# Kernel optimization log

Hardware: AMD Instinct MI355X
Metric: run time of the kernel (lower is better)

## Reference

```python
import jax, jax.numpy as jnp
import numpy as np

N, E, T = 10000, 160000, 1200000
D, DM, H, L, Z = 256, 64, 1024, 3, 100


def setup_inputs() -> dict:
    key = jax.random.key(0)
    ks = jax.random.split(key, 24)
    rn = lambda k, shp, s: (s * jax.random.normal(k, shp)).astype(jnp.float32)
    return {
        'atomic_number': jax.random.randint(ks[0], (N,), 1, Z),
        'g_src': jax.random.randint(ks[1], (E,), 0, N),
        'g_dst': jax.random.randint(ks[2], (E,), 0, N),
        't_src': jax.random.randint(ks[3], (T,), 0, E),
        't_dst': jax.random.randint(ks[4], (T,), 0, E),
        'r': rn(ks[5], (E, 3), 1.5),  # bond displacement vectors, |r| ~ 2.4 A
        'atom_emb': rn(ks[6], (Z, D), 0.05),
        'Wsrc': rn(ks[7], (L, D, DM), 0.05), 'bsrc': rn(ks[8], (L, DM), 0.05),
        'Wdst': rn(ks[9], (L, D, DM), 0.05), 'bdst': rn(ks[10], (L, DM), 0.05),
        'Wedge': rn(ks[11], (L, D, DM), 0.05), 'bedge': rn(ks[12], (L, DM), 0.05),
        'attn': rn(ks[13], (L, DM), 0.05),
        'W1': rn(ks[14], (L, DM, H), 0.05), 'b1': rn(ks[15], (L, H), 0.05),
        'W2': rn(ks[16], (L, H, D), 0.05), 'b2': rn(ks[17], (L, D), 0.05),
        'Wfc': rn(ks[18], (D, 1), 0.05), 'bfc': rn(ks[19], (1,), 0.05),
    }


def _forward(atomic_number, g_src, g_dst, t_src, t_dst, r, atom_emb,
             Wsrc, bsrc, Wdst, bdst, Wedge, bedge, attn, W1, b1, W2, b2, Wfc, bfc):
    n_nodes = atomic_number.shape[0]
    n_edges = r.shape[0]
    d_model = atom_emb.shape[1]
    channels = attn.shape[-1]

    # atom embedding + RBF bond encoding (vmin=0, vmax=8, bins=d_model)
    x = atom_emb[atomic_number]                       # [N, D]
    bondlength = jnp.linalg.norm(r, axis=1)           # [E]
    centers = jnp.linspace(0.0, 8.0, d_model)
    gamma = 1.0 / (centers[1] - centers[0]) ** 2
    y = jnp.exp(-gamma * (bondlength[:, None] - centers[None, :]) ** 2)  # [E, D]

    # angular (Chebyshev) features on triplet graph t; t.ndata['r'] = g.edata['r']
    rnorm = -r / bondlength[:, None]                  # [E, 3]
    cos_jik = jnp.sum(rnorm[t_src] * rnorm[t_dst], axis=1)  # [T]
    kc = jnp.arange(channels, dtype=cos_jik.dtype)
    theta = jnp.arccos(jnp.clip(cos_jik, -1.0, 1.0))
    z_jik = jnp.cos(kc[None, :] * theta[:, None])     # [T, C] Chebyshev T_k(cos)

    node_idx = g_dst[t_dst]                           # triplet -> destination atom

    for l in range(Wsrc.shape[0]):
        xj = x @ Wsrc[l] + bsrc[l]                    # [N, DM]
        xi = x @ Wdst[l] + bdst[l]                    # [N, DM]
        xij = xj[g_src] + xi[g_dst] + (y @ Wedge[l] + bedge[l])  # [E, DM]

        e_jik = jax.nn.silu(z_jik + xij[t_src] + xij[t_dst])     # [T, DM]
        logit = jnp.sum(e_jik * attn[l], axis=-1)                # [T]
        # edge_softmax grouped by destination bond (t_dst)
        m = jax.ops.segment_max(logit, t_dst, num_segments=n_edges)
        ex = jnp.exp(logit - m[t_dst])
        den = jax.ops.segment_sum(ex, t_dst, num_segments=n_edges)
        a = ex / den[t_dst]                                      # [T]

        # scatter attended messages to destination atoms
        ft = jax.ops.segment_sum(a[:, None] * xij[t_src], node_idx,
                                 num_segments=n_nodes)           # [N, DM]
        # feedforward: DM -> 4*D -> D
        x = jax.nn.silu(ft @ W1[l] + b1[l]) @ W2[l] + b2[l]      # [N, D]

    atomwise_energy = x @ Wfc + bfc                   # [N, 1]
    return jnp.squeeze(jnp.mean(atomwise_energy))     # AvgPooling, eV/atom


def reference(atomic_number, g_src, g_dst, t_src, t_dst, r, atom_emb,
              Wsrc, bsrc, Wdst, bdst, Wedge, bedge, attn, W1, b1, W2, b2, Wfc, bfc):
    return _forward(atomic_number, g_src, g_dst, t_src, t_dst, r, atom_emb,
                    Wsrc, bsrc, Wdst, bdst, Wedge, bedge, attn, W1, b1, W2, b2, Wfc, bfc)
```

## Files before the change

kernel.cpp:

```cpp
#include <hip/hip_runtime.h>
#include <math.h>


#define DM 64
#define DMODEL 256
#define HDIM 1024
#define WPAD 264

#define BSH 9
#define NBMAX 320
#define CAPB 4608

typedef unsigned short bf16_t;
typedef __attribute__((ext_vector_type(8))) short s8v;
typedef __attribute__((ext_vector_type(4))) float f4;

__device__ __forceinline__ bf16_t f2bf(float f) {
    unsigned int u = __float_as_uint(f);
    return (bf16_t)((u + 0x7FFFu + ((u >> 16) & 1u)) >> 16);
}
__device__ __forceinline__ float bf_lo(unsigned int u) {
    return __uint_as_float(u << 16);
}
__device__ __forceinline__ float bf_hi(unsigned int u) {
    return __uint_as_float(u & 0xFFFF0000u);
}
__device__ __forceinline__ float bf2f(bf16_t v) {
    return __uint_as_float((unsigned int)v << 16);
}
__device__ __forceinline__ float silu_f(float u) {
    return u * __builtin_amdgcn_rcpf(1.f + __expf(-u));
}

__global__ void k_embed(const int* __restrict__ an, const float* __restrict__ emb,
                        bf16_t* __restrict__ x) {
    int n = blockIdx.x;
    int d = threadIdx.x;
    x[n * DMODEL + d] = f2bf(emb[an[n] * DMODEL + d]);
}

__global__ void k_edge_geom(const float* __restrict__ r, float* __restrict__ bl,
                            float* __restrict__ rn, int E) {
    int e = blockIdx.x * blockDim.x + threadIdx.x;
    if (e >= E) return;
    float a = r[e * 3 + 0], b = r[e * 3 + 1], c = r[e * 3 + 2];
    float l = sqrtf(a * a + b * b + c * c);
    bl[e] = l;
    float inv = 1.0f / l;
    rn[e * 3 + 0] = a * inv;
    rn[e * 3 + 1] = b * inv;
    rn[e * 3 + 2] = c * inv;
}

__global__ void k_hist(const int* __restrict__ idx, int* __restrict__ cnt, int M) {
    int t = blockIdx.x * blockDim.x + threadIdx.x;
    if (t < M) atomicAdd(&cnt[idx[t]], 1);
}

__global__ __launch_bounds__(256) void k_scan_part(
    const int* __restrict__ cnt, int* __restrict__ bsum, int M) {
    __shared__ int sm[4];
    int tid = threadIdx.x;
    int i = blockIdx.x * 256 + tid;
    int v = (i < M) ? cnt[i] : 0;
    for (int off = 32; off > 0; off >>= 1) v += __shfl_xor(v, off, 64);
    if ((tid & 63) == 0) sm[tid >> 6] = v;
    __syncthreads();
    if (tid == 0) bsum[blockIdx.x] = sm[0] + sm[1] + sm[2] + sm[3];
}

__global__ __launch_bounds__(1024) void k_scan_mid(int* __restrict__ bsum, int nb) {
    __shared__ int sm[1024];
    int tid = threadIdx.x;
    int v = (tid < nb) ? bsum[tid] : 0;
    sm[tid] = v;
    __syncthreads();
    for (int off = 1; off < 1024; off <<= 1) {
        int u = (tid >= off) ? sm[tid - off] : 0;
        __syncthreads();
        sm[tid] += u;
        __syncthreads();
    }
    if (tid < nb) bsum[tid] = sm[tid] - v;
}

__global__ __launch_bounds__(256) void k_scan_final(
    const int* __restrict__ cnt, const int* __restrict__ bsum,
    int* __restrict__ rowp, int M, int total) {
    __shared__ int sm[256];
    int tid = threadIdx.x;
    int i = blockIdx.x * 256 + tid;
    int v = (i < M) ? cnt[i] : 0;
    sm[tid] = v;
    __syncthreads();
    for (int off = 1; off < 256; off <<= 1) {
        int u = (tid >= off) ? sm[tid - off] : 0;
        __syncthreads();
        sm[tid] += u;
        __syncthreads();
    }
    if (i < M) rowp[i] = bsum[blockIdx.x] + sm[tid] - v;
    if (i == 0) rowp[M] = total;
}


__global__ __launch_bounds__(512) void k_bhist(
    const int* __restrict__ td, int* __restrict__ gbcnt, int T, int NB) {
    __shared__ int h[NBMAX];
    int tid = threadIdx.x;
    for (int i = tid; i < NBMAX; i += 512) h[i] = 0;
    __syncthreads();
    int t0 = blockIdx.x * 4096;
    #pragma unroll
    for (int i = 0; i < 8; ++i) {
        int t = t0 + tid + i * 512;
        if (t < T) atomicAdd(&h[td[t] >> BSH], 1);
    }
    __syncthreads();
    for (int b = tid; b < NB; b += 512)
        if (h[b]) atomicAdd(&gbcnt[b], h[b]);
}

__global__ __launch_bounds__(512) void k_bscan(
    const int* __restrict__ gbcnt, int* __restrict__ bbase, int NB, int total) {
    __shared__ int sm[512];
    int tid = threadIdx.x;
    int v = (tid < NB) ? gbcnt[tid] : 0;
    sm[tid] = v;
    __syncthreads();
    for (int off = 1; off < 512; off <<= 1) {
        int u = (tid >= off) ? sm[tid - off] : 0;
        __syncthreads();
        sm[tid] += u;
        __syncthreads();
    }
    if (tid < NB) bbase[tid] = sm[tid] - v;
    if (tid == 0) bbase[NB] = total;
}

__global__ __launch_bounds__(512) void k_passA(
    const int* __restrict__ ts, const int* __restrict__ td,
    const float* __restrict__ rn, const int* __restrict__ bbase,
    int* __restrict__ bcur, int2* __restrict__ ipair, float* __restrict__ idv,
    int T, int NB) {
    __shared__ int   std_[4096];
    __shared__ int   ssrc[4096];
    __shared__ float sdv[4096];
    __shared__ int lbcnt[NBMAX], lbase[NBMAX], lpos[NBMAX], lgst[NBMAX],
                   lbb[NBMAX];
    __shared__ int ssc[512];
    int tid = threadIdx.x;
    int t0 = blockIdx.x * 4096;
    int total = min(4096, T - t0);
    for (int i = tid; i < NBMAX; i += 512) lbcnt[i] = 0;
    for (int i = tid; i < NB; i += 512) lbb[i] = bbase[i];
    __syncthreads();
    int   mtd[8], msrc[8];
    float md[8];
    #pragma unroll
    for (int i = 0; i < 8; ++i) {
        int idx = tid + i * 512;
        mtd[i] = -1;
        if (idx < total) {
            int t = t0 + idx;
            int a = ts[t], b = td[t];
            float d = rn[a * 3 + 0] * rn[b * 3 + 0]
                    + rn[a * 3 + 1] * rn[b * 3 + 1]
                    + rn[a * 3 + 2] * rn[b * 3 + 2];
            d = fminf(1.0f, fmaxf(-1.0f, d));
            mtd[i] = b; msrc[i] = a; md[i] = d;
            atomicAdd(&lbcnt[b >> BSH], 1);
        }
    }
    __syncthreads();
    int v = (tid < NB) ? lbcnt[tid] : 0;
    ssc[tid] = v;
    __syncthreads();
    for (int off = 1; off < 512; off <<= 1) {
        int u = (tid >= off) ? ssc[tid - off] : 0;
        __syncthreads();
        ssc[tid] += u;
        __syncthreads();
    }
    if (tid < NB) {
        int ex = ssc[tid] - v;
        lbase[tid] = ex;
        lpos[tid] = ex;
    }
    __syncthreads();
    #pragma unroll
    for (int i = 0; i < 8; ++i) {
        if (mtd[i] >= 0) {
            int bin = mtd[i] >> BSH;
            int p = atomicAdd(&lpos[bin], 1);
            std_[p] = mtd[i]; ssrc[p] = msrc[i]; sdv[p] = md[i];
        }
    }
    __syncthreads();
    for (int b = tid; b < NB; b += 512)
        if (lbcnt[b]) lgst[b] = atomicAdd(&bcur[b], lbcnt[b]);
    __syncthreads();
    for (int j = tid; j < total; j += 512) {
        int bin = std_[j] >> BSH;
        int dest = lbb[bin] + lgst[bin] + (j - lbase[bin]);
        ipair[dest] = make_int2(std_[j], ssrc[j]);
        idv[dest] = sdv[j];
    }
}

__global__ __launch_bounds__(512) void k_passB(
    const int2* __restrict__ ipair, const float* __restrict__ idv,
    const int* __restrict__ bbase, int2* __restrict__ packed,
    int* __restrict__ rowp, int E, int T) {
    __shared__ int2 spk[CAPB];
    __shared__ int hcnt[512], lcur[512], ssc[512];
    int tid = threadIdx.x;
    int b = blockIdx.x;
    int ibeg = bbase[b], iend = bbase[b + 1];
    int nb = iend - ibeg;
    int e0 = b << BSH;
    hcnt[tid] = 0;
    __syncthreads();
    for (int j = ibeg + tid; j < iend; j += 512)
        atomicAdd(&hcnt[ipair[j].x - e0], 1);
    __syncthreads();
    int v = hcnt[tid];
    ssc[tid] = v;
    __syncthreads();
    for (int off = 1; off < 512; off <<= 1) {
        int u = (tid >= off) ? ssc[tid - off] : 0;
        __syncthreads();
        ssc[tid] += u;
        __syncthreads();
    }
    int excl = ssc[tid] - v;
    lcur[tid] = excl;
    int e = e0 + tid;
    if (e < E) rowp[e] = ibeg + excl;
    if (b == 0 && tid == 0) rowp[E] = T;
    __syncthreads();
    bool staged = (nb <= CAPB);
    for (int j = ibeg + tid; j < iend; j += 512) {
        int2 pr = ipair[j];
        int pos = atomicAdd(&lcur[pr.x - e0], 1);
        int2 out = make_int2(pr.y, __float_as_int(idv[j]));
        if (staged) spk[pos] = out;
        else packed[ibeg + pos] = out;
    }
    __syncthreads();
    if (staged)
        for (int j = tid; j < nb; j += 512) packed[ibeg + j] = spk[j];
}

__global__ void k_escatter(const int* __restrict__ gd, const int* __restrict__ erowp,
                           int* __restrict__ cursor, int* __restrict__ eord, int E) {
    int e = blockIdx.x * blockDim.x + threadIdx.x;
    if (e >= E) return;
    int n = gd[e];
    int pos = erowp[n] + atomicAdd(&cursor[n], 1);
    eord[pos] = e;
}

__global__ __launch_bounds__(256) void k_deghist(
    const int* __restrict__ rowp, int* __restrict__ dcnt, int E) {
    __shared__ int h[256];
    int tid = threadIdx.x;
    h[tid] = 0;
    __syncthreads();
    int e = blockIdx.x * 256 + tid;
    if (e < E) {
        int d = rowp[e + 1] - rowp[e];
        if (d > 255) d = 255;
        atomicAdd(&h[d], 1);
    }
    __syncthreads();
    if (h[tid]) atomicAdd(&dcnt[tid], h[tid]);
}

__global__ __launch_bounds__(256) void k_degscatter(
    const int* __restrict__ rowp, const int* __restrict__ doff,
    int* __restrict__ dcur, int* __restrict__ eperm, int E) {
    __shared__ int lcnt[256];
    __shared__ int base[256];
    int tid = threadIdx.x;
    lcnt[tid] = 0;
    __syncthreads();
    int e = blockIdx.x * 256 + tid;
    int d = 0, rk = 0;
    if (e < E) {
        d = rowp[e + 1] - rowp[e];
        if (d > 255) d = 255;
        rk = atomicAdd(&lcnt[d], 1);
    }
    __syncthreads();
    if (lcnt[tid]) base[tid] = atomicAdd(&dcur[tid], lcnt[tid]);
    __syncthreads();
    if (e < E) eperm[E - 1 - (doff[d] + base[d] + rk)] = e;
}

__global__ __launch_bounds__(256) void k_castT(
    const float* __restrict__ src, bf16_t* __restrict__ dst, int K, int Nn) {
    __shared__ float tile[32][33];
    int k0 = blockIdx.x * 32, n0 = blockIdx.y * 32;
    int tx = threadIdx.x & 31, ty = threadIdx.x >> 5;
    #pragma unroll
    for (int i = 0; i < 4; ++i) {
        int row = ty + i * 8;
        tile[row][tx] = src[(size_t)(k0 + row) * Nn + n0 + tx];
    }
    __syncthreads();
    #pragma unroll
    for (int i = 0; i < 4; ++i) {
        int row = ty + i * 8;
        dst[(size_t)(n0 + row) * K + k0 + tx] = f2bf(tile[tx][row]);
    }
}

__global__ __launch_bounds__(256) void k_node_proj(
    const bf16_t* __restrict__ xb,
    const bf16_t* __restrict__ Wst, const float* __restrict__ bs,
    const bf16_t* __restrict__ Wdt, const float* __restrict__ bd,
    bf16_t* __restrict__ xs, bf16_t* __restrict__ xd, int N) {
    __shared__ bf16_t wsl[64 * WPAD];
    __shared__ bf16_t wdl[64 * WPAD];
    int tid = threadIdx.x;
    for (int i = tid; i < 2048; i += 256) {
        int row = i >> 5, inw = i & 31;
        *(uint4*)&wsl[row * WPAD + inw * 8] =
            *(const uint4*)&Wst[(size_t)row * DMODEL + inw * 8];
        *(uint4*)&wdl[row * WPAD + inw * 8] =
            *(const uint4*)&Wdt[(size_t)row * DMODEL + inw * 8];
    }
    __syncthreads();
    int w = tid >> 6, lane = tid & 63;
    int col = lane & 15, quad = lane >> 4;
    int m0 = blockIdx.x * 64 + w * 16;
    f4 as[4] = {{0.f,0.f,0.f,0.f},{0.f,0.f,0.f,0.f},
                {0.f,0.f,0.f,0.f},{0.f,0.f,0.f,0.f}};
    f4 ad[4] = {{0.f,0.f,0.f,0.f},{0.f,0.f,0.f,0.f},
                {0.f,0.f,0.f,0.f},{0.f,0.f,0.f,0.f}};
    #pragma unroll
    for (int k0 = 0; k0 < DMODEL; k0 += 32) {
        s8v a = *(const s8v*)&xb[(size_t)(m0 + col) * DMODEL + k0 + quad * 8];
        #pragma unroll
        for (int t = 0; t < 4; ++t) {
            s8v b1v = *(const s8v*)&wsl[(t * 16 + col) * WPAD + k0 + quad * 8];
            as[t] = __builtin_amdgcn_mfma_f32_16x16x32_bf16(a, b1v, as[t], 0, 0, 0);
            s8v b2v = *(const s8v*)&wdl[(t * 16 + col) * WPAD + k0 + quad * 8];
            ad[t] = __builtin_amdgcn_mfma_f32_16x16x32_bf16(a, b2v, ad[t], 0, 0, 0);
        }
    }
    #pragma unroll
    for (int t = 0; t < 4; ++t) {
        int c = t * 16 + col;
        float bsv = bs[c], bdv = bd[c];
        #pragma unroll
        for (int r = 0; r < 4; ++r) {
            int m = m0 + quad * 4 + r;
            if (m < N) {
                xs[(size_t)m * DM + c] = f2bf(as[t][r] + bsv);
                xd[(size_t)m * DM + c] = f2bf(ad[t][r] + bdv);
            }
        }
    }
}

__global__ __launch_bounds__(256) void k_xij(
    const float* __restrict__ bl, const bf16_t* __restrict__ Wedgt,
    const float* __restrict__ be,
    const bf16_t* __restrict__ xs, const bf16_t* __restrict__ xd,
    const int* __restrict__ gs, const int* __restrict__ gd,
    bf16_t* __restrict__ xij, int E) {
    __shared__ bf16_t wel[64 * WPAD];
    int tid = threadIdx.x;
    for (int i = tid; i < 2048; i += 256) {
        int row = i >> 5, inw = i & 31;
        *(uint4*)&wel[row * WPAD + inw * 8] =
            *(const uint4*)&Wedgt[(size_t)row * DMODEL + inw * 8];
    }
    __syncthreads();
    int w = tid >> 6, lane = tid & 63;
    int col = lane & 15, quad = lane >> 4;
    int m0 = blockIdx.x * 64 + w * 16;
    const float step = 8.0f / 255.0f;
    const float gamma = (255.0f / 8.0f) * (255.0f / 8.0f);
    int me = m0 + col;
    float blv = (me < E) ? bl[me] : 0.f;
    f4 acc[4] = {{0.f,0.f,0.f,0.f},{0.f,0.f,0.f,0.f},
                 {0.f,0.f,0.f,0.f},{0.f,0.f,0.f,0.f}};
    #pragma unroll
    for (int k0 = 0; k0 < DMODEL; k0 += 32) {
        s8v a;
        #pragma unroll
        for (int j = 0; j < 8; ++j) {
            float c = (float)(k0 + quad * 8 + j) * step;
            float dd = blv - c;
            a[j] = (short)f2bf(__expf(-gamma * dd * dd));
        }
        #pragma unroll
        for (int t = 0; t < 4; ++t) {
            s8v b = *(const s8v*)&wel[(t * 16 + col) * WPAD + k0 + quad * 8];
            acc[t] = __builtin_amdgcn_mfma_f32_16x16x32_bf16(a, b, acc[t], 0, 0, 0);
        }
    }
    #pragma unroll
    for (int r = 0; r < 4; ++r) {
        int e = m0 + quad * 4 + r;
        if (e >= E) continue;
        int s = gs[e], d2 = gd[e];
        #pragma unroll
        for (int t = 0; t < 4; ++t) {
            int c = t * 16 + col;
            float v = acc[t][r] + bf2f(xs[(size_t)s * DM + c])
                    + bf2f(xd[(size_t)d2 * DM + c]) + be[c];
            xij[(size_t)e * DM + c] = f2bf(v);
        }
    }
}

__global__ __launch_bounds__(256) void k_edge_attn(
    const bf16_t* __restrict__ xij, const int2* __restrict__ packed,
    const int* __restrict__ rowp, const float* __restrict__ attn_l,
    const int* __restrict__ eperm, bf16_t* __restrict__ msg, int E) {
    int gtid = blockIdx.x * 256 + threadIdx.x;
    int ei = gtid >> 2;
    if (ei >= E) return;
    int q = gtid & 3;
    int e = eperm[ei];
    int beg = rowp[e], end = rowp[e + 1];

    float av[16];
    #pragma unroll
    for (int c = 0; c < 16; ++c) av[c] = attn_l[q * 16 + c];

    uint4 xe0, xe1;
    {
        const uint4* xer = (const uint4*)&xij[(size_t)e * DM + q * 16];
        xe0 = xer[0]; xe1 = xer[1];
    }
    float acc[16];
    #pragma unroll
    for (int c = 0; c < 16; ++c) acc[c] = 0.f;
    float den = 0.f;

    int degw = __builtin_amdgcn_readfirstlane(end - beg);
    if (degw > 9) __builtin_amdgcn_s_setprio(1);

    if (beg < end) {
        int2 pk0 = packed[beg];
        int2 pk1 = (beg + 1 < end) ? packed[beg + 1] : pk0;
        const uint4* s0 = (const uint4*)&xij[(size_t)pk0.x * DM + q * 16];
        uint4 nsa = s0[0], nsb = s0[1];
        for (int p = beg; p < end; ++p) {
            float d = __int_as_float(pk0.y);
            uint4 xa = nsa, xb = nsb;
            if (p + 1 < end) {
                const uint4* sn = (const uint4*)&xij[(size_t)pk1.x * DM + q * 16];
                nsa = sn[0]; nsb = sn[1];
                pk0 = pk1;
                if (p + 2 < end) pk1 = packed[p + 2];
            }
            float d2 = d + d;
            float t2  = fmaf(d2, d, -1.f);
            float t3  = fmaf(d2, t2, -d);
            float t4  = fmaf(t2 + t2, t2, -1.f);
            float t7  = fmaf(t4 + t4, t3, -d);
            float t8  = fmaf(t4 + t4, t4, -1.f);
            float t15 = fmaf(t8 + t8, t7, -d);
            float t16 = fmaf(t8 + t8, t8, -1.f);
            float t17 = fmaf(t16 + t16, d, -t15);
            float t31 = fmaf(t16 + t16, t15, -d);
            float t32 = fmaf(t16 + t16, t16, -1.f);
            float t33 = fmaf(t32 + t32, d, -t31);
            float t48 = fmaf(t32 + t32, t16, -t16);
            float t49 = fmaf(t32 + t32, t17, -t15);
            float za, zb;
            if (q == 0)      { za = 1.f;  zb = d;   }
            else if (q == 1) { za = t16;  zb = t17; }
            else if (q == 2) { za = t32;  zb = t33; }
            else             { za = t48;  zb = t49; }
            float logit = 0.f;
            #define CH2(uw, ew, c)                                            \
            {                                                                 \
                float u0 = za + bf_lo(uw) + bf_lo(ew);                        \
                float zn = fmaf(d2, zb, -za); za = zb; zb = zn;               \
                float u1 = za + bf_hi(uw) + bf_hi(ew);                        \
                zn = fmaf(d2, zb, -za); za = zb; zb = zn;                     \
                logit = fmaf(silu_f(u0), av[c], logit);                       \
                logit = fmaf(silu_f(u1), av[c + 1], logit);                   \
            }
            CH2(xa.x, xe0.x, 0);
            CH2(xa.y, xe0.y, 2);
            CH2(xa.z, xe0.z, 4);
            CH2(xa.w, xe0.w, 6);
            CH2(xb.x, xe1.x, 8);
            CH2(xb.y, xe1.y, 10);
            CH2(xb.z, xe1.z, 12);
            CH2(xb.w, xe1.w, 14);
            #undef CH2
            logit += __shfl_xor(logit, 1, 64);
            logit += __shfl_xor(logit, 2, 64);
            float wg = __expf(logit);
            den += wg;
            acc[0]  = fmaf(wg, bf_lo(xa.x), acc[0]);
            acc[1]  = fmaf(wg, bf_hi(xa.x), acc[1]);
            acc[2]  = fmaf(wg, bf_lo(xa.y), acc[2]);
            acc[3]  = fmaf(wg, bf_hi(xa.y), acc[3]);
            acc[4]  = fmaf(wg, bf_lo(xa.z), acc[4]);
            acc[5]  = fmaf(wg, bf_hi(xa.z), acc[5]);
            acc[6]  = fmaf(wg, bf_lo(xa.w), acc[6]);
            acc[7]  = fmaf(wg, bf_hi(xa.w), acc[7]);
            acc[8]  = fmaf(wg, bf_lo(xb.x), acc[8]);
            acc[9]  = fmaf(wg, bf_hi(xb.x), acc[9]);
            acc[10] = fmaf(wg, bf_lo(xb.y), acc[10]);
            acc[11] = fmaf(wg, bf_hi(xb.y), acc[11]);
            acc[12] = fmaf(wg, bf_lo(xb.z), acc[12]);
            acc[13] = fmaf(wg, bf_hi(xb.z), acc[13]);
            acc[14] = fmaf(wg, bf_lo(xb.w), acc[14]);
            acc[15] = fmaf(wg, bf_hi(xb.w), acc[15]);
        }
    }
    __builtin_amdgcn_s_setprio(0);
    float inv = (den > 0.f) ? 1.f / den : 0.f;
    uint4 o0, o1;
    o0.x = (unsigned int)f2bf(acc[0] * inv)  | ((unsigned int)f2bf(acc[1] * inv) << 16);
    o0.y = (unsigned int)f2bf(acc[2] * inv)  | ((unsigned int)f2bf(acc[3] * inv) << 16);
    o0.z = (unsigned int)f2bf(acc[4] * inv)  | ((unsigned int)f2bf(acc[5] * inv) << 16);
    o0.w = (unsigned int)f2bf(acc[6] * inv)  | ((unsigned int)f2bf(acc[7] * inv) << 16);
    o1.x = (unsigned int)f2bf(acc[8] * inv)  | ((unsigned int)f2bf(acc[9] * inv) << 16);
    o1.y = (unsigned int)f2bf(acc[10] * inv) | ((unsigned int)f2bf(acc[11] * inv) << 16);
    o1.z = (unsigned int)f2bf(acc[12] * inv) | ((unsigned int)f2bf(acc[13] * inv) << 16);
    o1.w = (unsigned int)f2bf(acc[14] * inv) | ((unsigned int)f2bf(acc[15] * inv) << 16);
    uint4* op = (uint4*)&msg[(size_t)e * DM + q * 16];
    op[0] = o0;
    op[1] = o1;
}

__global__ __launch_bounds__(256) void k_aggregate(
    const bf16_t* __restrict__ msg, const int* __restrict__ erowp,
    const int* __restrict__ eord, bf16_t* __restrict__ ft, int N) {
    int gtid = blockIdx.x * 256 + threadIdx.x;
    int n = gtid >> 4;
    if (n >= N) return;
    int quad = gtid & 15;
    int beg = erowp[n], end = erowp[n + 1];
    float a0 = 0.f, a1 = 0.f, a2 = 0.f, a3 = 0.f;
    for (int j = beg; j < end; ++j) {
        uint2 uv = *(const uint2*)&msg[(size_t)eord[j] * DM + quad * 4];
        a0 += bf_lo(uv.x); a1 += bf_hi(uv.x);
        a2 += bf_lo(uv.y); a3 += bf_hi(uv.y);
    }
    ushort4 o = {f2bf(a0), f2bf(a1), f2bf(a2), f2bf(a3)};
    *(ushort4*)&ft[(size_t)n * DM + quad * 4] = o;
}

__global__ __launch_bounds__(256) void k_ffn_fused(
    const bf16_t* __restrict__ ft, const bf16_t* __restrict__ W1t,
    const float* __restrict__ b1, const bf16_t* __restrict__ W2t,
    const float* __restrict__ b2, bf16_t* __restrict__ x, int N) {
    __shared__ bf16_t w1s[2][64 * 72];
    __shared__ bf16_t w2s[2][64 * 72];
    __shared__ bf16_t hld[4][16 * 72];
    __shared__ float b1s[HDIM];
    int tid = threadIdx.x;
    int w = tid >> 6, lane = tid & 63;
    int col = lane & 15, quad = lane >> 4;
    int m0 = blockIdx.x * 64 + w * 16;
    int c0 = blockIdx.y * 64;
    bf16_t* myl = hld[w];

    #pragma unroll
    for (int j = 0; j < 4; ++j) b1s[tid + j * 256] = b1[tid + j * 256];

    s8v fa0 = *(const s8v*)&ft[(size_t)(m0 + col) * DM + quad * 8];
    s8v fa1 = *(const s8v*)&ft[(size_t)(m0 + col) * DM + 32 + quad * 8];

    int srow0 = tid >> 3;
    int srow1 = 32 + srow0;
    int skb = tid & 7;

    f4 acc[4] = {{0.f,0.f,0.f,0.f},{0.f,0.f,0.f,0.f},
                 {0.f,0.f,0.f,0.f},{0.f,0.f,0.f,0.f}};

    {
        uint4 a0 = *(const uint4*)&W1t[(size_t)srow0 * DM + skb * 8];
        uint4 a1 = *(const uint4*)&W1t[(size_t)srow1 * DM + skb * 8];
        uint4 c0v = *(const uint4*)&W2t[(size_t)(c0 + srow0) * HDIM + skb * 8];
        uint4 c1v = *(const uint4*)&W2t[(size_t)(c0 + srow1) * HDIM + skb * 8];
        *(uint4*)&w1s[0][srow0 * 72 + skb * 8] = a0;
        *(uint4*)&w1s[0][srow1 * 72 + skb * 8] = a1;
        *(uint4*)&w2s[0][srow0 * 72 + skb * 8] = c0v;
        *(uint4*)&w2s[0][srow1 * 72 + skb * 8] = c1v;
    }
    __syncthreads();

    #pragma unroll 1
    for (int kc = 0; kc < 16; ++kc) {
        int cb = kc & 1, nb = cb ^ 1;
        int ch0 = kc * 64;
        int chn = (kc < 15) ? ch0 + 64 : ch0;
        uint4 na0 = *(const uint4*)&W1t[(size_t)(chn + srow0) * DM + skb * 8];
        uint4 na1 = *(const uint4*)&W1t[(size_t)(chn + srow1) * DM + skb * 8];
        uint4 nc0 = *(const uint4*)&W2t[(size_t)(c0 + srow0) * HDIM + chn + skb * 8];
        uint4 nc1 = *(const uint4*)&W2t[(size_t)(c0 + srow1) * HDIM + chn + skb * 8];
        #pragma unroll
        for (int th = 0; th < 4; ++th) {
            s8v wb0 = *(const s8v*)&w1s[cb][(th * 16 + col) * 72 + quad * 8];
            s8v wb1 = *(const s8v*)&w1s[cb][(th * 16 + col) * 72 + 32 + quad * 8];
            f4 hv = {0.f, 0.f, 0.f, 0.f};
            hv = __builtin_amdgcn_mfma_f32_16x16x32_bf16(fa0, wb0, hv, 0, 0, 0);
            hv = __builtin_amdgcn_mfma_f32_16x16x32_bf16(fa1, wb1, hv, 0, 0, 0);
            float bb = b1s[ch0 + th * 16 + col];
            #pragma unroll
            for (int r = 0; r < 4; ++r)
                myl[(quad * 4 + r) * 72 + th * 16 + col] =
                    f2bf(silu_f(hv[r] + bb));
        }
        s8v ha0 = *(const s8v*)&myl[col * 72 + quad * 8];
        s8v ha1 = *(const s8v*)&myl[col * 72 + 32 + quad * 8];
        #pragma unroll
        for (int t2 = 0; t2 < 4; ++t2) {
            s8v vb0 = *(const s8v*)&w2s[cb][(t2 * 16 + col) * 72 + quad * 8];
            s8v vb1 = *(const s8v*)&w2s[cb][(t2 * 16 + col) * 72 + 32 + quad * 8];
            acc[t2] = __builtin_amdgcn_mfma_f32_16x16x32_bf16(ha0, vb0, acc[t2], 0, 0, 0);
            acc[t2] = __builtin_amdgcn_mfma_f32_16x16x32_bf16(ha1, vb1, acc[t2], 0, 0, 0);
        }
        __syncthreads();
        if (kc < 15) {
            *(uint4*)&w1s[nb][srow0 * 72 + skb * 8] = na0;
            *(uint4*)&w1s[nb][srow1 * 72 + skb * 8] = na1;
            *(uint4*)&w2s[nb][srow0 * 72 + skb * 8] = nc0;
            *(uint4*)&w2s[nb][srow1 * 72 + skb * 8] = nc1;
        }
        __syncthreads();
    }
    #pragma unroll
    for (int t2 = 0; t2 < 4; ++t2) {
        int c = c0 + t2 * 16 + col;
        float bb = b2[c];
        #pragma unroll
        for (int r = 0; r < 4; ++r) {
            int m = m0 + quad * 4 + r;
            if (m < N) x[(size_t)m * DMODEL + c] = f2bf(acc[t2][r] + bb);
        }
    }
}

__global__ __launch_bounds__(256) void k_out_reduce(
    const bf16_t* __restrict__ x, const float* __restrict__ Wfc,
    float* __restrict__ acc, int NT) {
    __shared__ float sm[4];
    int tid = threadIdx.x;
    float v = 0.f;
    int np = NT / 2;
    const unsigned int* xp = (const unsigned int*)x;
    for (int i = blockIdx.x * blockDim.x + tid; i < np; i += gridDim.x * blockDim.x) {
        unsigned int u = xp[i];
        int c = (2 * i) & (DMODEL - 1);
        v = fmaf(bf_lo(u), Wfc[c], v);
        v = fmaf(bf_hi(u), Wfc[c + 1], v);
    }
    for (int off = 32; off > 0; off >>= 1) v += __shfl_xor(v, off, 64);
    if ((tid & 63) == 0) sm[tid >> 6] = v;
    __syncthreads();
    if (tid == 0) {
        float s = sm[0] + sm[1] + sm[2] + sm[3];
        atomicAdd(acc, s);
    }
}

__global__ void k_out_final(const float* __restrict__ acc, const float* __restrict__ bfc,
                            float* __restrict__ out, float invN) {
    out[0] = acc[0] * invN + bfc[0];
}

extern "C" void kernel_launch(void* const* d_in, const int* in_sizes, int n_in,
                              void* d_out, int out_size, void* d_ws, size_t ws_size,
                              hipStream_t stream) {
    const int*   an    = (const int*)d_in[0];
    const int*   gs    = (const int*)d_in[1];
    const int*   gd    = (const int*)d_in[2];
    const int*   ts    = (const int*)d_in[3];
    const int*   td    = (const int*)d_in[4];
    const float* r     = (const float*)d_in[5];
    const float* emb   = (const float*)d_in[6];
    const float* Wsrc  = (const float*)d_in[7];
    const float* bsrc  = (const float*)d_in[8];
    const float* Wdst  = (const float*)d_in[9];
    const float* bdst  = (const float*)d_in[10];
    const float* Wedge = (const float*)d_in[11];
    const float* bedge = (const float*)d_in[12];
    const float* attn  = (const float*)d_in[13];
    const float* W1    = (const float*)d_in[14];
    const float* b1    = (const float*)d_in[15];
    const float* W2    = (const float*)d_in[16];
    const float* b2    = (const float*)d_in[17];
    const float* Wfc   = (const float*)d_in[18];
    const float* bfc   = (const float*)d_in[19];

    const int N = in_sizes[0];
    const int E = in_sizes[1];
    const int T = in_sizes[3];
    const int NB = (E + 511) >> BSH;

    char* w = (char*)d_ws;
    size_t off = 0;
    auto alloc = [&](size_t bytes) {
        void* p = w + off;
        off += (bytes + 255) & ~(size_t)255;
        return p;
    };
    bf16_t* xb     = (bf16_t*)alloc((size_t)(N + 64) * DMODEL * 2);
    float*  rn     = (float*) alloc((size_t)E * 3 * 4);
    float*  bl     = (float*) alloc(((size_t)E + 64) * 4);
    int*    rowp   = (int*)   alloc(((size_t)E + 1) * 4);
    int*    bsum   = (int*)   alloc(4096);
    int2*   packed = (int2*)  alloc((size_t)T * 8);
    int2*   ipair  = (int2*)  alloc((size_t)T * 8);
    float*  idv    = (float*) alloc((size_t)T * 4);
    int*    gbcnt  = (int*)   alloc(NBMAX * 4);
    int*    bbase  = (int*)   alloc((NBMAX + 1) * 4);
    int*    bcur   = (int*)   alloc(NBMAX * 4);
    int*    ecnt   = (int*)   alloc((size_t)N * 4);
    int*    erowp  = (int*)   alloc(((size_t)N + 1) * 4);
    int*    eord   = (int*)   alloc((size_t)E * 4);
    int*    eperm  = (int*)   alloc((size_t)E * 4);
    int*    dcnt   = (int*)   alloc(1024);
    int*    dcur   = (int*)   alloc(1024);
    bf16_t* xs     = (bf16_t*)alloc((size_t)N * DM * 2);
    bf16_t* xd     = (bf16_t*)alloc((size_t)N * DM * 2);
    bf16_t* xij    = (bf16_t*)alloc((size_t)E * DM * 2);
    bf16_t* msg    = (bf16_t*)alloc((size_t)E * DM * 2);
    bf16_t* ft     = (bf16_t*)alloc((size_t)(N + 64) * DM * 2);
    bf16_t* W1t    = (bf16_t*)alloc((size_t)3 * HDIM * DM * 2);
    bf16_t* W2t    = (bf16_t*)alloc((size_t)3 * DMODEL * HDIM * 2);
    bf16_t* Wedgt  = (bf16_t*)alloc((size_t)3 * DM * DMODEL * 2);
    bf16_t* Wst    = (bf16_t*)alloc((size_t)3 * DM * DMODEL * 2);
    bf16_t* Wdt    = (bf16_t*)alloc((size_t)3 * DM * DMODEL * 2);
    float*  accs   = (float*) alloc(64);
    (void)ws_size; (void)n_in; (void)out_size;

    const int nbScanN = (N + 255) / 256;
    const int nbT = (T + 4095) / 4096;

    k_embed<<<N, 256, 0, stream>>>(an, emb, xb);
    k_edge_geom<<<(E + 255) / 256, 256, 0, stream>>>(r, bl, rn, E);
    for (int l = 0; l < 3; ++l) {
        k_castT<<<dim3(DM / 32, HDIM / 32), 256, 0, stream>>>(
            W1 + (size_t)l * DM * HDIM, W1t + (size_t)l * HDIM * DM, DM, HDIM);
        k_castT<<<dim3(HDIM / 32, DMODEL / 32), 256, 0, stream>>>(
            W2 + (size_t)l * HDIM * DMODEL, W2t + (size_t)l * DMODEL * HDIM,
            HDIM, DMODEL);
        k_castT<<<dim3(DMODEL / 32, DM / 32), 256, 0, stream>>>(
            Wedge + (size_t)l * DMODEL * DM, Wedgt + (size_t)l * DM * DMODEL,
            DMODEL, DM);
        k_castT<<<dim3(DMODEL / 32, DM / 32), 256, 0, stream>>>(
            Wsrc + (size_t)l * DMODEL * DM, Wst + (size_t)l * DM * DMODEL,
            DMODEL, DM);
        k_castT<<<dim3(DMODEL / 32, DM / 32), 256, 0, stream>>>(
            Wdst + (size_t)l * DMODEL * DM, Wdt + (size_t)l * DM * DMODEL,
            DMODEL, DM);
    }
    hipMemsetAsync(gbcnt, 0, NBMAX * 4, stream);
    hipMemsetAsync(bcur, 0, NBMAX * 4, stream);
    k_bhist<<<nbT, 512, 0, stream>>>(td, gbcnt, T, NB);
    k_bscan<<<1, 512, 0, stream>>>(gbcnt, bbase, NB, T);
    k_passA<<<nbT, 512, 0, stream>>>(ts, td, rn, bbase, bcur, ipair, idv, T, NB);
    k_passB<<<NB, 512, 0, stream>>>(ipair, idv, bbase, packed, rowp, E, T);
    hipMemsetAsync(dcnt, 0, 1024, stream);
    hipMemsetAsync(dcur, 0, 1024, stream);
    k_deghist<<<(E + 255) / 256, 256, 0, stream>>>(rowp, dcnt, E);
    k_scan_mid<<<1, 1024, 0, stream>>>(dcnt, 256);
    k_degscatter<<<(E + 255) / 256, 256, 0, stream>>>(rowp, dcnt, dcur, eperm, E);
    hipMemsetAsync(ecnt, 0, (size_t)N * 4, stream);
    k_hist<<<(E + 255) / 256, 256, 0, stream>>>(gd, ecnt, E);
    k_scan_part<<<nbScanN, 256, 0, stream>>>(ecnt, bsum, N);
    k_scan_mid<<<1, 1024, 0, stream>>>(bsum, nbScanN);
    k_scan_final<<<nbScanN, 256, 0, stream>>>(ecnt, bsum, erowp, N, E);
    hipMemsetAsync(ecnt, 0, (size_t)N * 4, stream);
    k_escatter<<<(E + 255) / 256, 256, 0, stream>>>(gd, erowp, ecnt, eord, E);

    for (int l = 0; l < 3; ++l) {
        k_node_proj<<<(N + 63) / 64, 256, 0, stream>>>(
            xb, Wst + (size_t)l * DM * DMODEL, bsrc + l * DM,
            Wdt + (size_t)l * DM * DMODEL, bdst + l * DM, xs, xd, N);
        k_xij<<<(E + 63) / 64, 256, 0, stream>>>(
            bl, Wedgt + (size_t)l * DM * DMODEL, bedge + l * DM,
            xs, xd, gs, gd, xij, E);
        k_edge_attn<<<(E * 4 + 255) / 256, 256, 0, stream>>>(
            xij, packed, rowp, attn + l * DM, eperm, msg, E);
        k_aggregate<<<(N * 16 + 255) / 256, 256, 0, stream>>>(
            msg, erowp, eord, ft, N);
        k_ffn_fused<<<dim3((N + 63) / 64, 4), 256, 0, stream>>>(
            ft, W1t + (size_t)l * HDIM * DM, b1 + l * HDIM,
            W2t + (size_t)l * DMODEL * HDIM, b2 + l * DMODEL, xb, N);
    }

    hipMemsetAsync(accs, 0, 4, stream);
    k_out_reduce<<<120, 256, 0, stream>>>(xb, Wfc, accs, N * DMODEL);
    k_out_final<<<1, 1, 0, stream>>>(accs, bfc, (float*)d_out, 1.0f / (float)N);
}
```

Before: 635.3 us.

## Write edge messages in node-sorted order and batch setup launches

The edge attention kernel now writes each message directly to its destination-node-sorted slot (epos), so aggregation reads msg contiguously instead of gathering through eord. Weight cast launches are batched across layers with a z grid dimension, memsets are merged by reordering allocations to be adjacent, and scan_final zeroes the counters in place of a separate memset. The setprio hint for high-degree wavefronts in edge_attn is also removed. The attention writes become scattered while the aggregation reads become sequential.

```diff
diff --git a/kernel.cpp b/kernel.cpp
--- a/kernel.cpp
+++ b/kernel.cpp
@@ -85,7 +85,7 @@
 }
 
 __global__ __launch_bounds__(256) void k_scan_final(
-    const int* __restrict__ cnt, const int* __restrict__ bsum,
+    int* __restrict__ cnt, const int* __restrict__ bsum,
     int* __restrict__ rowp, int M, int total) {
     __shared__ int sm[256];
     int tid = threadIdx.x;
@@ -99,7 +99,10 @@
         sm[tid] += u;
         __syncthreads();
     }
-    if (i < M) rowp[i] = bsum[blockIdx.x] + sm[tid] - v;
+    if (i < M) {
+        rowp[i] = bsum[blockIdx.x] + sm[tid] - v;
+        cnt[i] = 0;
+    }
     if (i == 0) rowp[M] = total;
 }
 
@@ -253,12 +256,12 @@
 }
 
 __global__ void k_escatter(const int* __restrict__ gd, const int* __restrict__ erowp,
-                           int* __restrict__ cursor, int* __restrict__ eord, int E) {
+                           int* __restrict__ cursor, int* __restrict__ epos, int E) {
     int e = blockIdx.x * blockDim.x + threadIdx.x;
     if (e >= E) return;
     int n = gd[e];
     int pos = erowp[n] + atomicAdd(&cursor[n], 1);
-    eord[pos] = e;
+    epos[e] = pos;
 }
 
 __global__ __launch_bounds__(256) void k_deghist(
@@ -299,8 +302,10 @@
 }
 
 __global__ __launch_bounds__(256) void k_castT(
-    const float* __restrict__ src, bf16_t* __restrict__ dst, int K, int Nn) {
+    const float* __restrict__ src0, bf16_t* __restrict__ dst0, int K, int Nn) {
     __shared__ float tile[32][33];
+    const float* src = src0 + (size_t)blockIdx.z * K * Nn;
+    bf16_t* dst = dst0 + (size_t)blockIdx.z * K * Nn;
     int k0 = blockIdx.x * 32, n0 = blockIdx.y * 32;
     int tx = threadIdx.x & 31, ty = threadIdx.x >> 5;
     #pragma unroll
@@ -421,7 +426,8 @@
 __global__ __launch_bounds__(256) void k_edge_attn(
     const bf16_t* __restrict__ xij, const int2* __restrict__ packed,
     const int* __restrict__ rowp, const float* __restrict__ attn_l,
-    const int* __restrict__ eperm, bf16_t* __restrict__ msg, int E) {
+    const int* __restrict__ eperm, const int* __restrict__ epos,
+    bf16_t* __restrict__ msg, int E) {
     int gtid = blockIdx.x * 256 + threadIdx.x;
     int ei = gtid >> 2;
     if (ei >= E) return;
@@ -442,9 +448,6 @@
     #pragma unroll
     for (int c = 0; c < 16; ++c) acc[c] = 0.f;
     float den = 0.f;
-
-    int degw = __builtin_amdgcn_readfirstlane(end - beg);
-    if (degw > 9) __builtin_amdgcn_s_setprio(1);
 
     if (beg < end) {
         int2 pk0 = packed[beg];
@@ -520,7 +523,6 @@
             acc[15] = fmaf(wg, bf_hi(xb.w), acc[15]);
         }
     }
-    __builtin_amdgcn_s_setprio(0);
     float inv = (den > 0.f) ? 1.f / den : 0.f;
     uint4 o0, o1;
     o0.x = (unsigned int)f2bf(acc[0] * inv)  | ((unsigned int)f2bf(acc[1] * inv) << 16);
@@ -531,14 +533,15 @@
     o1.y = (unsigned int)f2bf(acc[10] * inv) | ((unsigned int)f2bf(acc[11] * inv) << 16);
     o1.z = (unsigned int)f2bf(acc[12] * inv) | ((unsigned int)f2bf(acc[13] * inv) << 16);
     o1.w = (unsigned int)f2bf(acc[14] * inv) | ((unsigned int)f2bf(acc[15] * inv) << 16);
-    uint4* op = (uint4*)&msg[(size_t)e * DM + q * 16];
+    int mrow = epos[e];
+    uint4* op = (uint4*)&msg[(size_t)mrow * DM + q * 16];
     op[0] = o0;
     op[1] = o1;
 }
 
 __global__ __launch_bounds__(256) void k_aggregate(
     const bf16_t* __restrict__ msg, const int* __restrict__ erowp,
-    const int* __restrict__ eord, bf16_t* __restrict__ ft, int N) {
+    bf16_t* __restrict__ ft, int N) {
     int gtid = blockIdx.x * 256 + threadIdx.x;
     int n = gtid >> 4;
     if (n >= N) return;
@@ -546,7 +549,7 @@
     int beg = erowp[n], end = erowp[n + 1];
     float a0 = 0.f, a1 = 0.f, a2 = 0.f, a3 = 0.f;
     for (int j = beg; j < end; ++j) {
-        uint2 uv = *(const uint2*)&msg[(size_t)eord[j] * DM + quad * 4];
+        uint2 uv = *(const uint2*)&msg[(size_t)j * DM + quad * 4];
         a0 += bf_lo(uv.x); a1 += bf_hi(uv.x);
         a2 += bf_lo(uv.y); a3 += bf_hi(uv.y);
     }
@@ -719,14 +722,14 @@
     int2*   ipair  = (int2*)  alloc((size_t)T * 8);
     float*  idv    = (float*) alloc((size_t)T * 4);
     int*    gbcnt  = (int*)   alloc(NBMAX * 4);
+    int*    bcur   = (int*)   alloc(NBMAX * 4);
     int*    bbase  = (int*)   alloc((NBMAX + 1) * 4);
-    int*    bcur   = (int*)   alloc(NBMAX * 4);
+    int*    dcnt   = (int*)   alloc(1024);
+    int*    dcur   = (int*)   alloc(1024);
     int*    ecnt   = (int*)   alloc((size_t)N * 4);
     int*    erowp  = (int*)   alloc(((size_t)N + 1) * 4);
-    int*    eord   = (int*)   alloc((size_t)E * 4);
+    int*    epos   = (int*)   alloc((size_t)E * 4);
     int*    eperm  = (int*)   alloc((size_t)E * 4);
-    int*    dcnt   = (int*)   alloc(1024);
-    int*    dcur   = (int*)   alloc(1024);
     bf16_t* xs     = (bf16_t*)alloc((size_t)N * DM * 2);
     bf16_t* xd     = (bf16_t*)alloc((size_t)N * DM * 2);
     bf16_t* xij    = (bf16_t*)alloc((size_t)E * DM * 2);
@@ -745,30 +748,17 @@
 
     k_embed<<<N, 256, 0, stream>>>(an, emb, xb);
     k_edge_geom<<<(E + 255) / 256, 256, 0, stream>>>(r, bl, rn, E);
-    for (int l = 0; l < 3; ++l) {
-        k_castT<<<dim3(DM / 32, HDIM / 32), 256, 0, stream>>>(
-            W1 + (size_t)l * DM * HDIM, W1t + (size_t)l * HDIM * DM, DM, HDIM);
-        k_castT<<<dim3(HDIM / 32, DMODEL / 32), 256, 0, stream>>>(
-            W2 + (size_t)l * HDIM * DMODEL, W2t + (size_t)l * DMODEL * HDIM,
-            HDIM, DMODEL);
-        k_castT<<<dim3(DMODEL / 32, DM / 32), 256, 0, stream>>>(
-            Wedge + (size_t)l * DMODEL * DM, Wedgt + (size_t)l * DM * DMODEL,
-            DMODEL, DM);
-        k_castT<<<dim3(DMODEL / 32, DM / 32), 256, 0, stream>>>(
-            Wsrc + (size_t)l * DMODEL * DM, Wst + (size_t)l * DM * DMODEL,
-            DMODEL, DM);
-        k_castT<<<dim3(DMODEL / 32, DM / 32), 256, 0, stream>>>(
-            Wdst + (size_t)l * DMODEL * DM, Wdt + (size_t)l * DM * DMODEL,
-            DMODEL, DM);
-    }
-    hipMemsetAsync(gbcnt, 0, NBMAX * 4, stream);
-    hipMemsetAsync(bcur, 0, NBMAX * 4, stream);
+    k_castT<<<dim3(DM / 32, HDIM / 32, 3), 256, 0, stream>>>(W1, W1t, DM, HDIM);
+    k_castT<<<dim3(HDIM / 32, DMODEL / 32, 3), 256, 0, stream>>>(W2, W2t, HDIM, DMODEL);
+    k_castT<<<dim3(DMODEL / 32, DM / 32, 3), 256, 0, stream>>>(Wedge, Wedgt, DMODEL, DM);
+    k_castT<<<dim3(DMODEL / 32, DM / 32, 3), 256, 0, stream>>>(Wsrc, Wst, DMODEL, DM);
+    k_castT<<<dim3(DMODEL / 32, DM / 32, 3), 256, 0, stream>>>(Wdst, Wdt, DMODEL, DM);
+    hipMemsetAsync(gbcnt, 0, (size_t)2 * NBMAX * 4, stream);
     k_bhist<<<nbT, 512, 0, stream>>>(td, gbcnt, T, NB);
     k_bscan<<<1, 512, 0, stream>>>(gbcnt, bbase, NB, T);
     k_passA<<<nbT, 512, 0, stream>>>(ts, td, rn, bbase, bcur, ipair, idv, T, NB);
     k_passB<<<NB, 512, 0, stream>>>(ipair, idv, bbase, packed, rowp, E, T);
-    hipMemsetAsync(dcnt, 0, 1024, stream);
-    hipMemsetAsync(dcur, 0, 1024, stream);
+    hipMemsetAsync(dcnt, 0, 2048, stream);
     k_deghist<<<(E + 255) / 256, 256, 0, stream>>>(rowp, dcnt, E);
     k_scan_mid<<<1, 1024, 0, stream>>>(dcnt, 256);
     k_degscatter<<<(E + 255) / 256, 256, 0, stream>>>(rowp, dcnt, dcur, eperm, E);
@@ -777,8 +767,7 @@
     k_scan_part<<<nbScanN, 256, 0, stream>>>(ecnt, bsum, N);
     k_scan_mid<<<1, 1024, 0, stream>>>(bsum, nbScanN);
     k_scan_final<<<nbScanN, 256, 0, stream>>>(ecnt, bsum, erowp, N, E);
-    hipMemsetAsync(ecnt, 0, (size_t)N * 4, stream);
-    k_escatter<<<(E + 255) / 256, 256, 0, stream>>>(gd, erowp, ecnt, eord, E);
+    k_escatter<<<(E + 255) / 256, 256, 0, stream>>>(gd, erowp, ecnt, epos, E);
 
     for (int l = 0; l < 3; ++l) {
         k_node_proj<<<(N + 63) / 64, 256, 0, stream>>>(
@@ -788,9 +777,9 @@
             bl, Wedgt + (size_t)l * DM * DMODEL, bedge + l * DM,
             xs, xd, gs, gd, xij, E);
         k_edge_attn<<<(E * 4 + 255) / 256, 256, 0, stream>>>(
-            xij, packed, rowp, attn + l * DM, eperm, msg, E);
+            xij, packed, rowp, attn + l * DM, eperm, epos, msg, E);
         k_aggregate<<<(N * 16 + 255) / 256, 256, 0, stream>>>(
-            msg, erowp, eord, ft, N);
+            msg, erowp, ft, N);
         k_ffn_fused<<<dim3((N + 63) / 64, 4), 256, 0, stream>>>(
             ft, W1t + (size_t)l * HDIM * DM, b1 + l * HDIM,
             W2t + (size_t)l * DMODEL * HDIM, b2 + l * DMODEL, xb, N);
```

New measurement: 596.1 us. 6.2% less time.
